# Performance work log

Measured on AMD Instinct MI355X. Metric: run time of the kernel, lower is better.

## Reference

```python
import jax, jax.numpy as jnp
import numpy as np

N = 8192
IN_F = 512
OUT_F = 64
NEG_INF = -9e15

def setup_inputs() -> dict:
    key = jax.random.key(0)
    k1, k2, k3, k4 = jax.random.split(key, 4)
    node_features = jax.random.normal(k1, (N, IN_F), dtype=jnp.float32)
    adjacency_matrix = jax.random.randint(k2, (N, N), 0, 2, dtype=jnp.int32)
    # Xavier-uniform-like init (gain 1.414), scale irrelevant for correctness
    w_bound = 1.414 * np.sqrt(6.0 / (IN_F + OUT_F))
    a_bound = 1.414 * np.sqrt(6.0 / (2 * OUT_F + 1))
    weight_matrix = jax.random.uniform(k3, (IN_F, OUT_F), minval=-w_bound, maxval=w_bound, dtype=jnp.float32)
    attention_vector = jax.random.uniform(k4, (2 * OUT_F, 1), minval=-a_bound, maxval=a_bound, dtype=jnp.float32)
    return {
        "node_features": node_features,
        "adjacency_matrix": adjacency_matrix,
        "weight_matrix": weight_matrix,
        "attention_vector": attention_vector,
    }

def reference(node_features, adjacency_matrix, weight_matrix, attention_vector):
    # h: [N, F] transformed features
    h = node_features @ weight_matrix
    # score[i, j] = h[i] . a_left + h[j] . a_right
    a_left = attention_vector[:OUT_F, 0]   # [F]
    a_right = attention_vector[OUT_F:, 0]  # [F]
    scores = (h @ a_left)[:, None] + (h @ a_right)[None, :]  # [N, N]
    # NOTE: source defines leaky_relu but never applies it in forward — faithful omission.
    masked = jnp.where(adjacency_matrix > 0, scores, NEG_INF)
    attn = jax.nn.softmax(masked, axis=1)  # [N, N]
    # dropout p=0 / inference: no-op
    out = attn @ h  # [N, F]
    return jax.nn.elu(out)  # concat=True path
```

## Files before the change

kernel.cpp:

```cpp
#include <hip/hip_runtime.h>
#include <hip/hip_bf16.h>
#include <cstdint>

#define NN      8192
#define OF      64
#define KC      16
#define CW      512
#define ASTR    72
#define PSTR    65

#define OFF_HW  0
#define OFF_P   1310720

typedef __attribute__((ext_vector_type(8))) short  s16x8;
typedef __attribute__((ext_vector_type(4))) float  f32x4;

__device__ __forceinline__ unsigned short f2bf(float f) {
  unsigned int u = __float_as_uint(f);
  unsigned int r = (u + 0x7FFFu + ((u >> 16) & 1u)) >> 16;
  return (unsigned short)r;
}

__global__ __launch_bounds__(256) void k1_hw(const float* __restrict__ X,
                                             const float* __restrict__ W,
                                             const float* __restrict__ att,
                                             unsigned short* __restrict__ HW) {
  __shared__ float xs[16 * 516];
  __shared__ float ws[64 * 68];
  int t = threadIdx.x;
  int rb = blockIdx.x * 16;

  {
    const float4* src = (const float4*)(X + (size_t)rb * 512);
#pragma unroll
    for (int s = 0; s < 8; ++s) {
      int lid = s * 256 + t;
      int row = lid >> 7, kseg = lid & 127;
      *(float4*)&xs[row * 516 + kseg * 4] = src[row * 128 + kseg];
    }
  }

  int row = t >> 4, tx = t & 15;
  float4 acc = {0.f, 0.f, 0.f, 0.f};
  for (int kc = 0; kc < 8; ++kc) {
    __syncthreads();
#pragma unroll
    for (int s = 0; s < 4; ++s) {
      int lid = s * 256 + t;
      int k = lid >> 4, cs = lid & 15;
      *(float4*)&ws[k * 68 + cs * 4] =
          *(const float4*)(W + (size_t)(kc * 64 + k) * 64 + cs * 4);
    }
    __syncthreads();
#pragma unroll 16
    for (int k = 0; k < 64; ++k) {
      float x = xs[row * 516 + kc * 64 + k];
      float4 w4 = *(const float4*)&ws[k * 68 + tx * 4];
      acc.x += x * w4.x; acc.y += x * w4.y;
      acc.z += x * w4.z; acc.w += x * w4.w;
    }
  }

  float v = acc.x * att[64 + tx * 4]     + acc.y * att[64 + tx * 4 + 1] +
            acc.z * att[64 + tx * 4 + 2] + acc.w * att[64 + tx * 4 + 3];
#pragma unroll
  for (int m = 8; m > 0; m >>= 1) v += __shfl_xor(v, m, 64);
  float e = expf(v);

  int j = rb + row;
  unsigned short* hw = HW + j;
  float hv[4] = {acc.x, acc.y, acc.z, acc.w};
#pragma unroll
  for (int c = 0; c < 4; ++c)
    hw[(size_t)(tx * 4 + c) * NN] = f2bf(e * hv[c]);
  if (tx == 0) hw[(size_t)64 * NN] = f2bf(e);
}

__global__ __launch_bounds__(256, 2) void k3_gat(const int* __restrict__ A,
                                                 const unsigned short* __restrict__ HW,
                                                 float* __restrict__ P) {
  __shared__ unsigned short bt[65 * 512];
  __shared__ unsigned short at[64 * ASTR];

  int t = threadIdx.x;
  int kc = blockIdx.x & 15;
  int mg = blockIdx.x >> 4;
  int lane = t & 63, w = t >> 6;
  int l15 = lane & 15, q = lane >> 4;
  int k0 = kc * CW;
  int rowM = mg * 64;

  const int* ap[4];
#pragma unroll
  for (int i = 0; i < 4; ++i)
    ap[i] = A + (size_t)(rowM + w * 16 + i * 4 + q) * NN + k0 + l15 * 4;

  int4 av[8][4];
#pragma unroll
  for (int s = 0; s < 8; ++s)
#pragma unroll
    for (int i = 0; i < 4; ++i)
      av[s][i] = *(const int4*)(ap[i] + s * 64);

#pragma unroll
  for (int rds = 0; rds < 16; ++rds) {
    int lid = rds * 256 + t;
    int row = lid >> 6, ch = lid & 63;
    uint4 v = *(const uint4*)(HW + (size_t)row * NN + k0 + ch * 8);
    *(uint4*)&bt[row * 512 + ((ch ^ (row & 7)) * 8)] = v;
  }
  if (t < 64) {
    uint4 v = *(const uint4*)(HW + (size_t)64 * NN + k0 + t * 8);
    *(uint4*)&bt[64 * 512 + t * 8] = v;
  }
  __syncthreads();

  int swz = l15 & 7;
  int bb[4][2];
#pragma unroll
  for (int tt = 0; tt < 4; ++tt)
#pragma unroll
    for (int ks = 0; ks < 2; ++ks)
      bb[tt][ks] = ((tt * 16 + l15) * 512 + (((ks * 4 + q) ^ swz) * 8)) * 2;
  int eb0 = (64 * 512 + q * 8) * 2;
  int eb1 = (64 * 512 + (4 + q) * 8) * 2;
  int ab  = ((w * 16 + l15) * ASTR + q * 8) * 2;

  f32x4 acc[5];
#pragma unroll
  for (int tt = 0; tt < 5; ++tt) acc[tt] = 0.f;
  const s16x8 zero8 = {0, 0, 0, 0, 0, 0, 0, 0};

#pragma unroll
  for (int s = 0; s < 8; ++s) {
#pragma unroll
    for (int i = 0; i < 4; ++i) {
      int4 vv = av[s][i];
      uint2 p;
      p.x = (unsigned)(vv.x | (vv.y << 16)) * 0x3F80u;
      p.y = (unsigned)(vv.z | (vv.w << 16)) * 0x3F80u;
      *(uint2*)((char*)at + (((w * 16 + i * 4 + q) * ASTR + l15 * 4) * 2)) = p;
    }

    s16x8 af0 = *(const s16x8*)((char*)at + ab);
    s16x8 af1 = *(const s16x8*)((char*)at + ab + 64);
    int so = s * 128;
#pragma unroll
    for (int ks = 0; ks < 2; ++ks) {
      s16x8 af = ks ? af1 : af0;
#pragma unroll
      for (int tt = 0; tt < 4; ++tt) {
        s16x8 b = *(const s16x8*)((char*)bt + bb[tt][ks] + so);
        acc[tt] = __builtin_amdgcn_mfma_f32_16x16x32_bf16(af, b, acc[tt], 0, 0, 0);
      }
      s16x8 b4 = *(const s16x8*)((char*)bt + (ks ? eb1 : eb0) + so);
      b4 = (l15 == 0) ? b4 : zero8;
      acc[4] = __builtin_amdgcn_mfma_f32_16x16x32_bf16(af, b4, acc[4], 0, 0, 0);
    }
  }

  float* Pp = P + (size_t)kc * NN * PSTR;
  int rb = rowM + w * 16 + q * 4;
#pragma unroll
  for (int tt = 0; tt < 4; ++tt)
#pragma unroll
    for (int rg = 0; rg < 4; ++rg)
      Pp[(size_t)(rb + rg) * PSTR + tt * 16 + l15] = acc[tt][rg];
  if (l15 == 0)
#pragma unroll
    for (int rg = 0; rg < 4; ++rg)
      Pp[(size_t)(rb + rg) * PSTR + 64] = acc[4][rg];
}

__global__ __launch_bounds__(256) void k4_fin(const float* __restrict__ P,
                                              float* __restrict__ out) {
  int g = blockIdx.x * 256 + threadIdx.x;
  int i = g >> 6, c = g & 63;
  float num = 0.f, S = 0.f;
#pragma unroll
  for (int kc = 0; kc < KC; ++kc) {
    const float* p = P + (size_t)kc * NN * PSTR + (size_t)i * PSTR;
    num += p[c];
    S   += p[64];
  }
  float x = num / S;
  out[g] = x > 0.f ? x : expm1f(x);
}

extern "C" void kernel_launch(void* const* d_in, const int* in_sizes, int n_in,
                              void* d_out, int out_size, void* d_ws, size_t ws_size,
                              hipStream_t stream) {
  const float* X  = (const float*)d_in[0];
  const int*   A  = (const int*)d_in[1];
  const float* W  = (const float*)d_in[2];
  const float* av = (const float*)d_in[3];
  float* out = (float*)d_out;

  char* ws = (char*)d_ws;
  unsigned short* HW = (unsigned short*)(ws + OFF_HW);
  float*          P  = (float*)(ws + OFF_P);

  k1_hw<<<NN / 16, 256, 0, stream>>>(X, W, av, HW);
  k3_gat<<<128 * KC, 256, 0, stream>>>(A, HW, P);
  k4_fin<<<(size_t)NN * OF / 256, 256, 0, stream>>>(P, out);
}
```

Measured before the change: 391.8 us.

## Compute feature projection with split-bf16 MFMA instead of scalar FP32 FMAs

The X@W projection kernel now uses bf16 MFMA instructions with a hi/lo split of both operands (three MFMAs per tile) to keep near-FP32 accuracy. A new single-block kernel pre-splits and transposes W into swizzled bf16 hi/lo buffers in workspace, and k1 converts X tiles on the fly into swizzled LDS. It aims to cut the scalar FMA cost of the projection, but adds an extra launch and a one-block serial prep kernel, and k1 is a small part of total time, which is dominated by the adjacency-stream kernel.

```diff
diff --git a/kernel.cpp b/kernel.cpp
--- a/kernel.cpp
+++ b/kernel.cpp
@@ -11,6 +11,7 @@
 
 #define OFF_HW  0
 #define OFF_P   1310720
+#define OFF_WT  35389440
 
 typedef __attribute__((ext_vector_type(8))) short  s16x8;
 typedef __attribute__((ext_vector_type(4))) float  f32x4;
@@ -21,59 +22,134 @@
   return (unsigned short)r;
 }
 
-__global__ __launch_bounds__(256) void k1_hw(const float* __restrict__ X,
-                                             const float* __restrict__ W,
+__global__ __launch_bounds__(256) void k0_wt(const float* __restrict__ W,
+                                             unsigned short* __restrict__ WT) {
+  int t = threadIdx.x;
+  int c = t & 63, part = t >> 6;
+  unsigned short* wh = WT;
+  unsigned short* wl = WT + 4 * 64 * 128;
+#pragma unroll 1
+  for (int kg = 0; kg < 16; ++kg) {
+    s16x8 hh, ll;
+#pragma unroll
+    for (int j = 0; j < 8; ++j) {
+      float x = W[(size_t)(part * 128 + kg * 8 + j) * 64 + c];
+      unsigned short h = f2bf(x);
+      float hf = __uint_as_float(((unsigned int)h) << 16);
+      hh[j] = (short)h;
+      ll[j] = (short)f2bf(x - hf);
+    }
+    size_t o = (size_t)part * 8192 + c * 128 + ((kg ^ (c & 7)) * 8);
+    *(s16x8*)(wh + o) = hh;
+    *(s16x8*)(wl + o) = ll;
+  }
+}
+
+__global__ __launch_bounds__(128) void k1_hw(const float* __restrict__ X,
+                                             const unsigned short* __restrict__ WT,
                                              const float* __restrict__ att,
                                              unsigned short* __restrict__ HW) {
-  __shared__ float xs[16 * 516];
-  __shared__ float ws[64 * 68];
+  __shared__ unsigned short xh[16 * 128], xl[16 * 128];
+  __shared__ unsigned short wh[64 * 128], wl[64 * 128];
+  __shared__ float vbuf[2][16];
+
   int t = threadIdx.x;
+  int lane = t & 63, w = t >> 6;
+  int l15 = lane & 15, q = lane >> 4;
   int rb = blockIdx.x * 16;
-
-  {
-    const float4* src = (const float4*)(X + (size_t)rb * 512);
-#pragma unroll
-    for (int s = 0; s < 8; ++s) {
-      int lid = s * 256 + t;
-      int row = lid >> 7, kseg = lid & 127;
-      *(float4*)&xs[row * 516 + kseg * 4] = src[row * 128 + kseg];
-    }
-  }
-
-  int row = t >> 4, tx = t & 15;
-  float4 acc = {0.f, 0.f, 0.f, 0.f};
-  for (int kc = 0; kc < 8; ++kc) {
+  const unsigned short* WTl = WT + 4 * 64 * 128;
+
+  f32x4 acc[2];
+  acc[0] = 0.f; acc[1] = 0.f;
+
+#pragma unroll 1
+  for (int kc = 0; kc < 4; ++kc) {
+    if (kc) __syncthreads();
+
+#pragma unroll
+    for (int i = 0; i < 8; ++i) {
+      int sl = (i * 128 + t) * 8;
+      *(s16x8*)&wh[sl] = *(const s16x8*)(WT  + (size_t)kc * 8192 + sl);
+      *(s16x8*)&wl[sl] = *(const s16x8*)(WTl + (size_t)kc * 8192 + sl);
+    }
+
+#pragma unroll
+    for (int i = 0; i < 4; ++i) {
+      int lid = i * 128 + t;
+      int row = lid >> 5, f4i = lid & 31;
+      float4 v = ((const float4*)X)[(size_t)(rb + row) * 128 + kc * 32 + f4i];
+      short4 hs, ls;
+      float xv[4] = {v.x, v.y, v.z, v.w};
+      short hv[4], lv[4];
+#pragma unroll
+      for (int j = 0; j < 4; ++j) {
+        unsigned short h = f2bf(xv[j]);
+        float hf = __uint_as_float(((unsigned int)h) << 16);
+        hv[j] = (short)h;
+        lv[j] = (short)f2bf(xv[j] - hf);
+      }
+      hs.x = hv[0]; hs.y = hv[1]; hs.z = hv[2]; hs.w = hv[3];
+      ls.x = lv[0]; ls.y = lv[1]; ls.z = lv[2]; ls.w = lv[3];
+      int kg = f4i >> 1, sub = (f4i & 1) * 4;
+      int col = ((kg ^ (row & 7)) * 8) + sub;
+      *(short4*)&xh[row * 128 + col] = hs;
+      *(short4*)&xl[row * 128 + col] = ls;
+    }
     __syncthreads();
-#pragma unroll
-    for (int s = 0; s < 4; ++s) {
-      int lid = s * 256 + t;
-      int k = lid >> 4, cs = lid & 15;
-      *(float4*)&ws[k * 68 + cs * 4] =
-          *(const float4*)(W + (size_t)(kc * 64 + k) * 64 + cs * 4);
-    }
-    __syncthreads();
-#pragma unroll 16
-    for (int k = 0; k < 64; ++k) {
-      float x = xs[row * 516 + kc * 64 + k];
-      float4 w4 = *(const float4*)&ws[k * 68 + tx * 4];
-      acc.x += x * w4.x; acc.y += x * w4.y;
-      acc.z += x * w4.z; acc.w += x * w4.w;
-    }
-  }
-
-  float v = acc.x * att[64 + tx * 4]     + acc.y * att[64 + tx * 4 + 1] +
-            acc.z * att[64 + tx * 4 + 2] + acc.w * att[64 + tx * 4 + 3];
-#pragma unroll
-  for (int m = 8; m > 0; m >>= 1) v += __shfl_xor(v, m, 64);
-  float e = expf(v);
-
-  int j = rb + row;
-  unsigned short* hw = HW + j;
-  float hv[4] = {acc.x, acc.y, acc.z, acc.w};
-#pragma unroll
-  for (int c = 0; c < 4; ++c)
-    hw[(size_t)(tx * 4 + c) * NN] = f2bf(e * hv[c]);
-  if (tx == 0) hw[(size_t)64 * NN] = f2bf(e);
+
+#pragma unroll
+    for (int ks = 0; ks < 4; ++ks) {
+      int ch = ks * 4 + q;
+      int acol = (ch ^ (l15 & 7)) * 8;
+      s16x8 afh = *(const s16x8*)&xh[l15 * 128 + acol];
+      s16x8 afl = *(const s16x8*)&xl[l15 * 128 + acol];
+#pragma unroll
+      for (int tti = 0; tti < 2; ++tti) {
+        int c = (w * 2 + tti) * 16 + l15;
+        int bcol = (ch ^ (l15 & 7)) * 8;
+        s16x8 bh = *(const s16x8*)&wh[c * 128 + bcol];
+        s16x8 bl = *(const s16x8*)&wl[c * 128 + bcol];
+        acc[tti] = __builtin_amdgcn_mfma_f32_16x16x32_bf16(afh, bh, acc[tti], 0, 0, 0);
+        acc[tti] = __builtin_amdgcn_mfma_f32_16x16x32_bf16(afl, bh, acc[tti], 0, 0, 0);
+        acc[tti] = __builtin_amdgcn_mfma_f32_16x16x32_bf16(afh, bl, acc[tti], 0, 0, 0);
+      }
+    }
+  }
+
+  float ar0 = att[64 + (w * 2 + 0) * 16 + l15];
+  float ar1 = att[64 + (w * 2 + 1) * 16 + l15];
+  float pv[4];
+#pragma unroll
+  for (int rg = 0; rg < 4; ++rg) {
+    float v = acc[0][rg] * ar0 + acc[1][rg] * ar1;
+#pragma unroll
+    for (int m = 8; m > 0; m >>= 1) v += __shfl_xor(v, m, 64);
+    pv[rg] = v;
+  }
+  if (l15 == 0) {
+#pragma unroll
+    for (int rg = 0; rg < 4; ++rg) vbuf[w][q * 4 + rg] = pv[rg];
+  }
+  __syncthreads();
+
+  float e[4];
+#pragma unroll
+  for (int rg = 0; rg < 4; ++rg)
+    e[rg] = expf(vbuf[0][q * 4 + rg] + vbuf[1][q * 4 + rg]);
+
+  int j0 = rb + q * 4;
+#pragma unroll
+  for (int tti = 0; tti < 2; ++tti) {
+    int c = (w * 2 + tti) * 16 + l15;
+#pragma unroll
+    for (int rg = 0; rg < 4; ++rg)
+      HW[(size_t)c * NN + j0 + rg] = f2bf(e[rg] * acc[tti][rg]);
+  }
+  if (w == 0 && l15 == 0) {
+#pragma unroll
+    for (int rg = 0; rg < 4; ++rg)
+      HW[(size_t)64 * NN + j0 + rg] = f2bf(e[rg]);
+  }
 }
 
 __global__ __launch_bounds__(256, 2) void k3_gat(const int* __restrict__ A,
@@ -199,8 +275,10 @@
   char* ws = (char*)d_ws;
   unsigned short* HW = (unsigned short*)(ws + OFF_HW);
   float*          P  = (float*)(ws + OFF_P);
-
-  k1_hw<<<NN / 16, 256, 0, stream>>>(X, W, av, HW);
+  unsigned short* WT = (unsigned short*)(ws + OFF_WT);
+
+  k0_wt<<<1, 256, 0, stream>>>(W, WT);
+  k1_hw<<<NN / 16, 128, 0, stream>>>(X, WT, av, HW);
   k3_gat<<<128 * KC, 256, 0, stream>>>(A, HW, P);
   k4_fin<<<(size_t)NN * OF / 256, 256, 0, stream>>>(P, out);
 }
```

Measured after the change: 397.2 us. Within noise of the previous version (+1.4%).
